# Optimization experiments

Measured on AMD Instinct MI355X. Metric: run time of the kernel, lower is better.

## Reference

```python
import jax, jax.numpy as jnp
import numpy as np

N, E, K_ORDER = 50000, 800000, 3
F_IN, H = 128, 128


def setup_inputs() -> dict:
    key = jax.random.key(0)
    ks = jax.random.split(key, 24)
    s = 0.05
    inp = {
        "x_t": jax.random.normal(ks[0], (N, F_IN), jnp.float32),
        "h_prev": jax.random.normal(ks[1], (N, H), jnp.float32),
        "c_prev": jax.random.normal(ks[2], (N, H), jnp.float32),
        "edge_weight": jax.random.uniform(ks[3], (E,), jnp.float32),
        "edge_index": jax.random.randint(ks[4], (2, E), 0, N, dtype=jnp.int64),
    }
    # Input->gate weight matrices W_* : (F, H)
    for i, nm in enumerate(["W_i", "W_f", "W_c", "W_o"]):
        inp[nm] = jax.random.normal(ks[5 + i], (F_IN, H), jnp.float32) * s
    # ChebConv weights theta_* : (K, H, H) applied to hidden state
    for i, nm in enumerate(["theta_i", "theta_f", "theta_c", "theta_o"]):
        inp[nm] = jax.random.normal(ks[9 + i], (K_ORDER, H, H), jnp.float32) * s
    # Gate biases (b_* of GCLSTM merged with the ChebConv bias; they add)
    for i, nm in enumerate(["b_i", "b_f", "b_c", "b_o"]):
        inp[nm] = jax.random.normal(ks[13 + i], (H,), jnp.float32) * s
    # Peephole weights w_c_* : (H,)
    for i, nm in enumerate(["w_ci", "w_cf", "w_co"]):
        inp[nm] = jax.random.normal(ks[17 + i], (H,), jnp.float32) * s
    return inp


def _cheb_norm(edge_index, edge_weight):
    # get_laplacian('sym') + lambda_max=2 scaling + add_self_loops(-1)
    # => L~ = -D^{-1/2} A D^{-1/2}  (zero diagonal)
    src, dst = edge_index[0], edge_index[1]
    deg = jax.ops.segment_sum(edge_weight, src, num_segments=N)
    dinv = jnp.where(deg > 0, jax.lax.rsqrt(jnp.maximum(deg, 1e-30)), 0.0)
    return src, dst, -edge_weight * dinv[src] * dinv[dst]


def _cheb_conv(x, theta, bias, src, dst, wn):
    # Chebyshev recursion: Tx0=x, Tx1=L~x, Tx_k = 2 L~ Tx_{k-1} - Tx_{k-2}
    def Lmul(v):
        return jax.ops.segment_sum(wn[:, None] * v[src], dst, num_segments=N)
    Tx0 = x
    Tx1 = Lmul(x)
    out = Tx0 @ theta[0] + Tx1 @ theta[1]
    for k in range(2, theta.shape[0]):
        Tx2 = 2.0 * Lmul(Tx1) - Tx0
        out = out + Tx2 @ theta[k]
        Tx0, Tx1 = Tx1, Tx2
    return out + bias


def reference(x_t, h_prev, c_prev, edge_weight, W_i, W_f, W_c, W_o,
              theta_i, theta_f, theta_c, theta_o, b_i, b_f, b_c, b_o,
              w_ci, w_cf, w_co, edge_index):
    src, dst, wn = _cheb_norm(edge_index, edge_weight)
    i = jax.nn.sigmoid(x_t @ W_i + _cheb_conv(h_prev, theta_i, b_i, src, dst, wn)
                       + w_ci * c_prev)
    f = jax.nn.sigmoid(x_t @ W_f + _cheb_conv(h_prev, theta_f, b_f, src, dst, wn)
                       + w_cf * c_prev)
    t = jnp.tanh(x_t @ W_c + _cheb_conv(h_prev, theta_c, b_c, src, dst, wn))
    c_t = f * c_prev + i * t
    o = jax.nn.sigmoid(x_t @ W_o + _cheb_conv(h_prev, theta_o, b_o, src, dst, wn)
                       + w_co * c_t)
    h_t = o * jnp.tanh(c_t)
    return (h_t, c_t)
```

## Files before the change

kernel.cpp:

```cpp
#include <hip/hip_runtime.h>

#define NN 50000
#define EE 800000
#define KC 64
#define EPC (EE / KC)
#define DEG_SCALE 4096.0f

typedef float f32x4 __attribute__((ext_vector_type(4)));
typedef short bf16x8 __attribute__((ext_vector_type(8)));
typedef unsigned short u16x8 __attribute__((ext_vector_type(8)));

__device__ __forceinline__ unsigned short f2bf(float f) {
  unsigned int u = __float_as_uint(f);
  u += 0x7fffu + ((u >> 16) & 1u);
  return (unsigned short)(u >> 16);
}
__device__ __forceinline__ float bf2f(unsigned short u) {
  return __uint_as_float(((unsigned int)u) << 16);
}

__device__ __forceinline__ void async_copy16(const void* g, void* l) {
  __builtin_amdgcn_global_load_lds(
      (const __attribute__((address_space(1))) unsigned int*)g,
      (__attribute__((address_space(3))) unsigned int*)l, 16, 0, 0);
}

__device__ __forceinline__ float fast_sig(float x) {
  return __builtin_amdgcn_rcpf(1.f + __expf(-x));
}
__device__ __forceinline__ float fast_tanh(float x) {
  return 1.f - 2.f * __builtin_amdgcn_rcpf(__expf(2.f * x) + 1.f);
}

__device__ __forceinline__ unsigned short* hslot2(char* o, long j) {
  return (unsigned short*)(o + (j >> 7) * 512 + (j & 127) * 2);
}
__device__ __forceinline__ void store8u16(char* o, long s, uint4 v) {
  *(uint4*)(o + (s >> 7) * 512 + (s & 127) * 2) = v;
}
#define CNT_SLOT0 3200000L
#define RANK_SLOT0 3200000L

__global__ __launch_bounds__(1024) void k_pre(
    const float* __restrict__ Wi, const float* __restrict__ Wf,
    const float* __restrict__ Wc, const float* __restrict__ Wo,
    const float* __restrict__ Ti, const float* __restrict__ Tf,
    const float* __restrict__ Tc, const float* __restrict__ To,
    unsigned short* __restrict__ bglob, const float* __restrict__ h,
    const float* __restrict__ x, char* __restrict__ outB,
    const int* __restrict__ src, const int* __restrict__ dst,
    const float* __restrict__ w) {
  __shared__ unsigned hist[25000];
  const int b = blockIdx.x, tid = threadIdx.x;
  char* cB = outB + (long)NN * 512;
  if (b < KC) {
    uint4* h4 = (uint4*)hist;
    const int base = b * EPC;
    for (int j = tid; j < 6250; j += 1024) h4[j] = (uint4){0u, 0u, 0u, 0u};
    __syncthreads();
    for (int k = tid; k < EPC; k += 1024) {
      const int e = base + k;
      const int d = dst[e];
      const int sh = (d & 1) * 16;
      const unsigned old = atomicAdd(&hist[d >> 1], 1u << sh);
      *hslot2(cB, RANK_SLOT0 + e) = (unsigned short)((old >> sh) & 0xffffu);
    }
    __syncthreads();
    for (int j = tid; j < 6250; j += 1024)
      store8u16(outB, CNT_SLOT0 + (long)b * NN + j * 8, h4[j]);
    __syncthreads();
    for (int j = tid; j < 6250; j += 1024) h4[j] = (uint4){0u, 0u, 0u, 0u};
    __syncthreads();
    for (int k = tid; k < EPC; k += 1024) {
      const int e = base + k;
      const int s = src[e];
      const unsigned q = (unsigned)__float2uint_rn(w[e] * DEG_SCALE);
      const int sh = (s & 1) * 16;
      atomicAdd(&hist[s >> 1], q << sh);
    }
    __syncthreads();
    for (int j = tid; j < 6250; j += 1024)
      store8u16(outB, (long)b * NN + j * 8, h4[j]);
  } else if (b < KC + 32) {
    const int t = (b - KC) * 1024 + tid;
    const int ks = t >> 11;
    const int cf = (t >> 6) & 31;
    const int lane = t & 63;
    const int wv = cf >> 3, hl = (cf >> 2) & 1, g = cf & 3;
    const int kg = lane >> 4, lm = lane & 15;
    const int hc = (wv * 2 + hl) * 16 + lm;
    const float* Wg = (g == 0) ? Wi : (g == 1) ? Wf : (g == 2) ? Wc : Wo;
    const float* Tg = (g == 0) ? Ti : (g == 1) ? Tf : (g == 2) ? Tc : To;
    u16x8 out;
#pragma unroll
    for (int dk = 0; dk < 8; ++dk) {
      const int k = ks * 32 + kg * 8 + dk;
      const int kb = k >> 7, r = k & 127;
      const float v = (kb == 0) ? Wg[r * 128 + hc] : Tg[(kb - 1) * 16384 + r * 128 + hc];
      out[dk] = f2bf(v);
    }
    *(u16x8*)(bglob + t * 8) = out;
  } else if (b < KC + 32 + 782) {
    const int i = (b - (KC + 32)) * 1024 + tid;
    if (i < 100000 * 8) {
      const float* hp = h + i * 8;
      const f32x4 v0 = *(const f32x4*)hp;
      const f32x4 v1 = *(const f32x4*)(hp + 4);
      u16x8 o;
#pragma unroll
      for (int e = 0; e < 4; ++e) o[e] = f2bf(v0[e]);
#pragma unroll
      for (int e = 0; e < 4; ++e) o[e + 4] = f2bf(v1[e]);
      *(u16x8*)(outB + (i >> 4) * 512 + 256 + (i & 15) * 16) = o;
    }
  } else {
    const int i = (b - (KC + 32 + 782)) * 1024 + tid;
    if (i < 100000 * 8) {
      const float* xp = x + i * 8;
      const f32x4 v0 = *(const f32x4*)xp;
      const f32x4 v1 = *(const f32x4*)(xp + 4);
      u16x8 o;
#pragma unroll
      for (int e = 0; e < 4; ++e) o[e] = f2bf(v0[e]);
#pragma unroll
      for (int e = 0; e < 4; ++e) o[e + 4] = f2bf(v1[e]);
      *(u16x8*)(cB + (i >> 4) * 512 + 256 + (i & 15) * 16) = o;
    }
  }
}

__global__ __launch_bounds__(256) void k_phase2(char* __restrict__ outB,
                                                float* __restrict__ dinv,
                                                int* __restrict__ wscnt) {
  char* cB = outB + (long)NN * 512;
  const int lane = threadIdx.x & 63;
  const int i = blockIdx.x * 4 + (threadIdx.x >> 6);
  const int c = lane;
  const int cnt_c = (int)*hslot2(outB, CNT_SLOT0 + (long)c * NN + i);
  const float deg_c = (float)*hslot2(outB, (long)c * NN + i);
  int x = cnt_c;
#pragma unroll
  for (int d = 1; d < 64; d <<= 1) {
    const int y = __shfl_up(x, d, 64);
    if (lane >= d) x += y;
  }
  *hslot2(cB, (long)c * NN + i) = (unsigned short)(x - cnt_c);
  float s = deg_c;
#pragma unroll
  for (int d = 1; d < 64; d <<= 1) s += __shfl_xor(s, d, 64);
  if (lane == 0) {
    s *= (1.0f / DEG_SCALE);
    dinv[i] = (s > 0.f) ? rsqrtf(fmaxf(s, 1e-30f)) : 0.f;
  }
  if (lane == 63) wscnt[i] = x;
}

__device__ __forceinline__ int block_scan_excl_256(int v, int* total) {
  __shared__ int wsum[4];
  const int tid = threadIdx.x;
  const int lane = tid & 63, wv = tid >> 6;
  int x = v;
#pragma unroll
  for (int d = 1; d < 64; d <<= 1) {
    const int y = __shfl_up(x, d, 64);
    if (lane >= d) x += y;
  }
  if (lane == 63) wsum[wv] = x;
  __syncthreads();
  int pre = 0, tot = 0;
#pragma unroll
  for (int u = 0; u < 4; ++u) {
    const int s = wsum[u];
    pre += (u < wv) ? s : 0;
    tot += s;
  }
  *total = tot;
  return pre + x - v;
}

__global__ void k_scan1(const int* __restrict__ wscnt, int* __restrict__ bsum) {
  const int i = blockIdx.x * 256 + threadIdx.x;
  const int v = (i < NN) ? wscnt[i] : 0;
  int tot;
  block_scan_excl_256(v, &tot);
  if (threadIdx.x == 0) bsum[blockIdx.x] = tot;
}

__global__ void k_scan2(const int* __restrict__ bsum, int* __restrict__ boff,
                        const int nb) {
  const int t = threadIdx.x;
  const int v = (t < nb) ? bsum[t] : 0;
  int tot;
  const int excl = block_scan_excl_256(v, &tot);
  if (t <= nb) boff[t] = excl;
}

__global__ void k_scan3(const int* __restrict__ cnt, const int* __restrict__ boff,
                        int* __restrict__ off) {
  const int i = blockIdx.x * 256 + threadIdx.x;
  const int v = (i < NN) ? cnt[i] : 0;
  int tot;
  const int excl = block_scan_excl_256(v, &tot) + boff[blockIdx.x];
  if (i < NN) off[i] = excl;
  if (i == NN) off[NN] = excl;
}

__global__ void k_edge2(const int* __restrict__ src, const int* __restrict__ dst,
                        const float* __restrict__ w, const float* __restrict__ dinv,
                        const int* __restrict__ off, char* __restrict__ outB,
                        int2* __restrict__ ed) {
  const int e = blockIdx.x * blockDim.x + threadIdx.x;
  if (e >= EE) return;
  char* cB = outB + (long)NN * 512;
  const int s = src[e], d = dst[e];
  const int c = e / EPC;
  const int p = off[d] + (int)*hslot2(cB, (long)c * NN + d) +
                (int)*hslot2(cB, RANK_SLOT0 + e);
  int2 rec;
  rec.x = s;
  rec.y = __float_as_int(-w[e] * dinv[s] * dinv[d]);
  ed[p] = rec;
}

__global__ __launch_bounds__(256) void k_gather(
    const char* __restrict__ vinB, const char* __restrict__ vsubB, const float alpha,
    const int* __restrict__ off, const int2* __restrict__ ed, char* __restrict__ voutB) {
  const int wid = threadIdx.x >> 6, lane = threadIdx.x & 63;
  const int node = blockIdx.x * 4 + wid;
  const int p0 = off[node], p1 = off[node + 1];
  const int lb = lane * 4;
  float ax0 = 0.f, ay0 = 0.f, ax1 = 0.f, ay1 = 0.f;
  float ax2 = 0.f, ay2 = 0.f, ax3 = 0.f, ay3 = 0.f;
  int p = p0;
  for (; p + 7 < p1; p += 8) {
    int2 E[8];
    unsigned V[8];
#pragma unroll
    for (int u = 0; u < 8; ++u) E[u] = ed[p + u];
#pragma unroll
    for (int u = 0; u < 8; ++u)
      V[u] = *(const unsigned*)(vinB + (long)E[u].x * 512 + lb);
#pragma unroll
    for (int u = 0; u < 8; ++u) {
      const float wv = __int_as_float(E[u].y);
      float* ax = (u & 3) == 0 ? &ax0 : (u & 3) == 1 ? &ax1 : (u & 3) == 2 ? &ax2 : &ax3;
      float* ay = (u & 3) == 0 ? &ay0 : (u & 3) == 1 ? &ay1 : (u & 3) == 2 ? &ay2 : &ay3;
      *ax = fmaf(wv, bf2f((unsigned short)V[u]), *ax);
      *ay = fmaf(wv, bf2f((unsigned short)(V[u] >> 16)), *ay);
    }
  }
  for (; p + 3 < p1; p += 4) {
    const int2 e0 = ed[p], e1 = ed[p + 1], e2 = ed[p + 2], e3 = ed[p + 3];
    const unsigned v0 = *(const unsigned*)(vinB + (long)e0.x * 512 + lb);
    const unsigned v1 = *(const unsigned*)(vinB + (long)e1.x * 512 + lb);
    const unsigned v2 = *(const unsigned*)(vinB + (long)e2.x * 512 + lb);
    const unsigned v3 = *(const unsigned*)(vinB + (long)e3.x * 512 + lb);
    const float w0 = __int_as_float(e0.y), w1 = __int_as_float(e1.y);
    const float w2 = __int_as_float(e2.y), w3 = __int_as_float(e3.y);
    ax0 = fmaf(w0, bf2f((unsigned short)v0), ax0);
    ay0 = fmaf(w0, bf2f((unsigned short)(v0 >> 16)), ay0);
    ax1 = fmaf(w1, bf2f((unsigned short)v1), ax1);
    ay1 = fmaf(w1, bf2f((unsigned short)(v1 >> 16)), ay1);
    ax2 = fmaf(w2, bf2f((unsigned short)v2), ax2);
    ay2 = fmaf(w2, bf2f((unsigned short)(v2 >> 16)), ay2);
    ax3 = fmaf(w3, bf2f((unsigned short)v3), ax3);
    ay3 = fmaf(w3, bf2f((unsigned short)(v3 >> 16)), ay3);
  }
  for (; p < p1; ++p) {
    const int2 e0 = ed[p];
    const unsigned v0 = *(const unsigned*)(vinB + (long)e0.x * 512 + lb);
    const float w0 = __int_as_float(e0.y);
    ax0 = fmaf(w0, bf2f((unsigned short)v0), ax0);
    ay0 = fmaf(w0, bf2f((unsigned short)(v0 >> 16)), ay0);
  }
  float rx = alpha * ((ax0 + ax1) + (ax2 + ax3));
  float ry = alpha * ((ay0 + ay1) + (ay2 + ay3));
  if (vsubB) {
    const unsigned s = *(const unsigned*)(vsubB + (long)node * 512 + lb);
    rx -= bf2f((unsigned short)s);
    ry -= bf2f((unsigned short)(s >> 16));
  }
  const unsigned ow = (unsigned)f2bf(rx) | ((unsigned)f2bf(ry) << 16);
  *(unsigned*)(voutB + (long)node * 512 + lb) = ow;
}

__global__ __launch_bounds__(512, 4) void k_gemm(
    const char* __restrict__ outB, const unsigned short* __restrict__ bglob,
    const float* __restrict__ c_prev,
    const float* __restrict__ b_i, const float* __restrict__ b_f,
    const float* __restrict__ b_c, const float* __restrict__ b_o,
    const float* __restrict__ w_ci, const float* __restrict__ w_cf,
    const float* __restrict__ w_co, float* __restrict__ h_out,
    float* __restrict__ c_out) {
  __shared__ char lds[65536];
  const int tid = threadIdx.x;
  const int lane = tid & 63;
  const int w = tid >> 6;
  const int kg = lane >> 4;
  const int lm = lane & 15;
  const int m0 = blockIdx.x * 64;

  const char* hB = outB;
  const char* cB = outB + (long)NN * 512;

  {
    const int t8 = tid & 255;
    const int rf = t8 >> 6, ln = t8 & 63;
    const int srow0 = m0 + rf * 16 + (ln & 15);
    const long srow = (srow0 < NN) ? srow0 : (NN - 1);
    const int schunk = (ln >> 4) * 16;
#pragma unroll
    for (int i = 0; i < 8; ++i) {
      const int ks = i * 2 + (tid >> 8);
      const char* base = (ks < 4) ? (cB + 256) : (ks < 8) ? (hB + 256) : (ks < 12) ? hB : cB;
      async_copy16(base + srow * 512 + (ks & 3) * 64 + schunk,
                   &lds[ks * 4096 + t8 * 16]);
    }
  }

  f32x4 acc[16];
#pragma unroll
  for (int i = 0; i < 16; ++i) acc[i] = (f32x4){0.f, 0.f, 0.f, 0.f};

  bf16x8 B[3][4];
  auto loadB = [&](int ks, bf16x8* bb) {
    const unsigned short* fp = bglob + ((ks * 32 + w * 4) * 64 + lane) * 8;
#pragma unroll
    for (int g = 0; g < 4; ++g) bb[g] = *(const bf16x8*)(fp + g * 512);
  };

  loadB(0, B[0]);
  loadB(1, B[1]);
  loadB(2, B[2]);

  __syncthreads();

#pragma unroll
  for (int ks = 0; ks < 16; ++ks) {
    const int m = ks % 3;
    bf16x8 a[4];
#pragma unroll
    for (int rf = 0; rf < 4; ++rf)
      a[rf] = *(const bf16x8*)(&lds[ks * 4096 + rf * 1024 + lane * 16]);
#pragma unroll
    for (int rf = 0; rf < 4; ++rf)
#pragma unroll
      for (int g = 0; g < 4; ++g)
        acc[rf * 4 + g] =
            __builtin_amdgcn_mfma_f32_16x16x32_bf16(a[rf], B[m][g], acc[rf * 4 + g], 0, 0, 0);
    if (ks + 3 < 16) loadB(ks + 3, B[m]);
  }

  const int hc = w * 16 + lm;
  const float bi = b_i[hc], bfv = b_f[hc], bc_ = b_c[hc], bo = b_o[hc];
  const float wci = w_ci[hc], wcf = w_cf[hc], wco = w_co[hc];
#pragma unroll
  for (int rf = 0; rf < 4; ++rf) {
#pragma unroll
    for (int reg = 0; reg < 4; ++reg) {
      const int node = m0 + rf * 16 + kg * 4 + reg;
      if (node < NN) {
        const float cp = c_prev[node * 128 + hc];
        const float pi = acc[rf * 4 + 0][reg] + bi + wci * cp;
        const float pf = acc[rf * 4 + 1][reg] + bfv + wcf * cp;
        const float pc = acc[rf * 4 + 2][reg] + bc_;
        const float po = acc[rf * 4 + 3][reg] + bo;
        const float ig = fast_sig(pi);
        const float fg = fast_sig(pf);
        const float ct = fg * cp + ig * fast_tanh(pc);
        const float og = fast_sig(po + wco * ct);
        h_out[node * 128 + hc] = og * fast_tanh(ct);
        c_out[node * 128 + hc] = ct;
      }
    }
  }
}


extern "C" void kernel_launch(void* const* d_in, const int* in_sizes, int n_in,
                              void* d_out, int out_size, void* d_ws, size_t ws_size,
                              hipStream_t stream) {
  const float* x_t    = (const float*)d_in[0];
  const float* h_prev = (const float*)d_in[1];
  const float* c_prev = (const float*)d_in[2];
  const float* ew     = (const float*)d_in[3];
  const int*   eidx   = (const int*)d_in[4];
  const float* Wi = (const float*)d_in[5];
  const float* Wf = (const float*)d_in[6];
  const float* Wc = (const float*)d_in[7];
  const float* Wo = (const float*)d_in[8];
  const float* Ti = (const float*)d_in[9];
  const float* Tf = (const float*)d_in[10];
  const float* Tc = (const float*)d_in[11];
  const float* To = (const float*)d_in[12];
  const float* bi = (const float*)d_in[13];
  const float* bf = (const float*)d_in[14];
  const float* bc = (const float*)d_in[15];
  const float* bo = (const float*)d_in[16];
  const float* wci = (const float*)d_in[17];
  const float* wcf = (const float*)d_in[18];
  const float* wco = (const float*)d_in[19];

  char* ws = (char*)d_ws;
  float* dinv  = (float*)(ws + 0);
  int*   wscnt = (int*)(ws + 200192);
  int*   off   = (int*)(ws + 400384);
  int*   bsum  = (int*)(ws + 601088);
  int*   boff  = (int*)(ws + 602112);
  int2*  ed    = (int2*)(ws + 603136);
  unsigned short* bglob = (unsigned short*)(ws + 7003136);

  char* outB = (char*)d_out;
  float* h_out = (float*)d_out;
  float* c_out = h_out + (long)NN * 128;

  const int* esrc = eidx;
  const int* edst = eidx + EE;

  k_pre<<<KC + 32 + 782 + 782, 1024, 0, stream>>>(
      Wi, Wf, Wc, Wo, Ti, Tf, Tc, To, bglob, h_prev, x_t, outB, esrc, edst, ew);
  k_phase2<<<12500, 256, 0, stream>>>(outB, dinv, wscnt);
  k_scan1<<<196, 256, 0, stream>>>(wscnt, bsum);
  k_scan2<<<1, 256, 0, stream>>>(bsum, boff, 196);
  k_scan3<<<196, 256, 0, stream>>>(wscnt, boff, off);
  k_edge2<<<3125, 256, 0, stream>>>(esrc, edst, ew, dinv, off, outB, ed);
  k_gather<<<12500, 256, 0, stream>>>(outB + 256, nullptr, 1.f, off, ed, outB);
  k_gather<<<12500, 256, 0, stream>>>(outB, outB + 256, 2.f, off, ed,
                                      outB + (long)NN * 512);
  k_gemm<<<782, 512, 0, stream>>>(outB, bglob, c_prev,
                                  bi, bf, bc, bo, wci, wcf, wco, h_out, c_out);
}
```

Baseline: 197.2 us.

## Make GEMM kernel persistent with double-buffered LDS panel prefetch

The gate GEMM/LSTM epilogue kernel becomes a persistent kernel: 256 blocks loop over the 782 row panels. While the current panel is being computed, the next panel's A tiles are staged asynchronously into a second 64KB LDS buffer. The A fragments are also double-buffered in registers across k-steps, and c_prev is prefetched before the MFMA loop. The aim is to hide global-to-LDS load latency and the tail of a partial wave. In exchange, LDS use doubles to 128KB per block, which limits occupancy to one block per CU, and the launch bound drops to 2.

```diff
diff --git a/kernel.cpp b/kernel.cpp
--- a/kernel.cpp
+++ b/kernel.cpp
@@ -5,6 +5,7 @@
 #define KC 64
 #define EPC (EE / KC)
 #define DEG_SCALE 4096.0f
+#define NPANEL 782
 
 typedef float f32x4 __attribute__((ext_vector_type(4)));
 typedef short bf16x8 __attribute__((ext_vector_type(8)));
@@ -284,7 +285,7 @@
   *(unsigned*)(voutB + (long)node * 512 + lb) = ow;
 }
 
-__global__ __launch_bounds__(512, 4) void k_gemm(
+__global__ __launch_bounds__(512, 2) void k_gemm(
     const char* __restrict__ outB, const unsigned short* __restrict__ bglob,
     const float* __restrict__ c_prev,
     const float* __restrict__ b_i, const float* __restrict__ b_f,
@@ -292,35 +293,32 @@
     const float* __restrict__ w_ci, const float* __restrict__ w_cf,
     const float* __restrict__ w_co, float* __restrict__ h_out,
     float* __restrict__ c_out) {
-  __shared__ char lds[65536];
+  __shared__ char lds[2][65536];
   const int tid = threadIdx.x;
   const int lane = tid & 63;
   const int w = tid >> 6;
   const int kg = lane >> 4;
   const int lm = lane & 15;
-  const int m0 = blockIdx.x * 64;
 
   const char* hB = outB;
   const char* cB = outB + (long)NN * 512;
 
-  {
-    const int t8 = tid & 255;
-    const int rf = t8 >> 6, ln = t8 & 63;
-    const int srow0 = m0 + rf * 16 + (ln & 15);
+  const int t8 = tid & 255;
+  const int sks0 = tid >> 8;
+  const int srowoff = (t8 >> 6) * 16 + (t8 & 15);
+  const int schunk = ((t8 & 63) >> 4) * 16;
+
+  auto stageA = [&](int p, int buf) {
+    const int srow0 = p * 64 + srowoff;
     const long srow = (srow0 < NN) ? srow0 : (NN - 1);
-    const int schunk = (ln >> 4) * 16;
 #pragma unroll
     for (int i = 0; i < 8; ++i) {
-      const int ks = i * 2 + (tid >> 8);
+      const int ks = i * 2 + sks0;
       const char* base = (ks < 4) ? (cB + 256) : (ks < 8) ? (hB + 256) : (ks < 12) ? hB : cB;
       async_copy16(base + srow * 512 + (ks & 3) * 64 + schunk,
-                   &lds[ks * 4096 + t8 * 16]);
-    }
-  }
-
-  f32x4 acc[16];
-#pragma unroll
-  for (int i = 0; i < 16; ++i) acc[i] = (f32x4){0.f, 0.f, 0.f, 0.f};
+                   &lds[buf][ks * 4096 + t8 * 16]);
+    }
+  };
 
   bf16x8 B[3][4];
   auto loadB = [&](int ks, bf16x8* bb) {
@@ -329,50 +327,78 @@
     for (int g = 0; g < 4; ++g) bb[g] = *(const bf16x8*)(fp + g * 512);
   };
 
-  loadB(0, B[0]);
-  loadB(1, B[1]);
-  loadB(2, B[2]);
-
-  __syncthreads();
-
-#pragma unroll
-  for (int ks = 0; ks < 16; ++ks) {
-    const int m = ks % 3;
-    bf16x8 a[4];
-#pragma unroll
-    for (int rf = 0; rf < 4; ++rf)
-      a[rf] = *(const bf16x8*)(&lds[ks * 4096 + rf * 1024 + lane * 16]);
-#pragma unroll
-    for (int rf = 0; rf < 4; ++rf)
-#pragma unroll
-      for (int g = 0; g < 4; ++g)
-        acc[rf * 4 + g] =
-            __builtin_amdgcn_mfma_f32_16x16x32_bf16(a[rf], B[m][g], acc[rf * 4 + g], 0, 0, 0);
-    if (ks + 3 < 16) loadB(ks + 3, B[m]);
-  }
-
   const int hc = w * 16 + lm;
   const float bi = b_i[hc], bfv = b_f[hc], bc_ = b_c[hc], bo = b_o[hc];
   const float wci = w_ci[hc], wcf = w_cf[hc], wco = w_co[hc];
-#pragma unroll
-  for (int rf = 0; rf < 4; ++rf) {
-#pragma unroll
-    for (int reg = 0; reg < 4; ++reg) {
-      const int node = m0 + rf * 16 + kg * 4 + reg;
-      if (node < NN) {
-        const float cp = c_prev[node * 128 + hc];
-        const float pi = acc[rf * 4 + 0][reg] + bi + wci * cp;
-        const float pf = acc[rf * 4 + 1][reg] + bfv + wcf * cp;
-        const float pc = acc[rf * 4 + 2][reg] + bc_;
-        const float po = acc[rf * 4 + 3][reg] + bo;
-        const float ig = fast_sig(pi);
-        const float fg = fast_sig(pf);
-        const float ct = fg * cp + ig * fast_tanh(pc);
-        const float og = fast_sig(po + wco * ct);
-        h_out[node * 128 + hc] = og * fast_tanh(ct);
-        c_out[node * 128 + hc] = ct;
+
+  int buf = 0;
+  stageA(blockIdx.x, 0);
+
+  for (int p = blockIdx.x; p < NPANEL; p += 256) {
+    __syncthreads();
+    if (p + 256 < NPANEL) stageA(p + 256, buf ^ 1);
+    const int m0 = p * 64;
+    float cp[16];
+#pragma unroll
+    for (int rf = 0; rf < 4; ++rf)
+#pragma unroll
+      for (int reg = 0; reg < 4; ++reg) {
+        int node = m0 + rf * 16 + kg * 4 + reg;
+        if (node >= NN) node = NN - 1;
+        cp[rf * 4 + reg] = c_prev[node * 128 + hc];
       }
-    }
+    loadB(0, B[0]);
+    loadB(1, B[1]);
+    loadB(2, B[2]);
+
+    f32x4 acc[16];
+#pragma unroll
+    for (int i = 0; i < 16; ++i) acc[i] = (f32x4){0.f, 0.f, 0.f, 0.f};
+
+    bf16x8 a0[4], a1[4];
+#pragma unroll
+    for (int rf = 0; rf < 4; ++rf)
+      a0[rf] = *(const bf16x8*)(&lds[buf][rf * 1024 + lane * 16]);
+#pragma unroll
+    for (int ks = 0; ks < 16; ++ks) {
+      bf16x8* ac = (ks & 1) ? a1 : a0;
+      bf16x8* an = (ks & 1) ? a0 : a1;
+      if (ks < 15) {
+#pragma unroll
+        for (int rf = 0; rf < 4; ++rf)
+          an[rf] = *(const bf16x8*)(&lds[buf][(ks + 1) * 4096 + rf * 1024 + lane * 16]);
+      }
+      const int m = ks % 3;
+#pragma unroll
+      for (int rf = 0; rf < 4; ++rf)
+#pragma unroll
+        for (int g = 0; g < 4; ++g)
+          acc[rf * 4 + g] = __builtin_amdgcn_mfma_f32_16x16x32_bf16(
+              ac[rf], B[m][g], acc[rf * 4 + g], 0, 0, 0);
+      if (ks + 3 < 16) loadB(ks + 3, B[m]);
+    }
+
+#pragma unroll
+    for (int rf = 0; rf < 4; ++rf) {
+#pragma unroll
+      for (int reg = 0; reg < 4; ++reg) {
+        const int node = m0 + rf * 16 + kg * 4 + reg;
+        if (node < NN) {
+          const float cpv = cp[rf * 4 + reg];
+          const float pi = acc[rf * 4 + 0][reg] + bi + wci * cpv;
+          const float pf = acc[rf * 4 + 1][reg] + bfv + wcf * cpv;
+          const float pc = acc[rf * 4 + 2][reg] + bc_;
+          const float po = acc[rf * 4 + 3][reg] + bo;
+          const float ig = fast_sig(pi);
+          const float fg = fast_sig(pf);
+          const float ct = fg * cpv + ig * fast_tanh(pc);
+          const float og = fast_sig(po + wco * ct);
+          h_out[node * 128 + hc] = og * fast_tanh(ct);
+          c_out[node * 128 + hc] = ct;
+        }
+      }
+    }
+    buf ^= 1;
   }
 }
 
@@ -427,6 +453,6 @@
   k_gather<<<12500, 256, 0, stream>>>(outB + 256, nullptr, 1.f, off, ed, outB);
   k_gather<<<12500, 256, 0, stream>>>(outB, outB + 256, 2.f, off, ed,
                                       outB + (long)NN * 512);
-  k_gemm<<<782, 512, 0, stream>>>(outB, bglob, c_prev,
+  k_gemm<<<256, 512, 0, stream>>>(outB, bglob, c_prev,
                                   bi, bf, bc, bo, wci, wcf, wco, h_out, c_out);
 }
```

Result: slower. 241.1 us (+22.3%).

## Redistribute h/x bf16 conversion into later kernels and deepen GEMM B prefetch

Applied to the files above, without the earlier changes.

Moves the h_prev bf16 conversion out of the histogram pre-kernel into extra blocks of k_phase2, and the x_t conversion into extra blocks of the first gather. The aim is to shorten the critical histogram kernel and fill idle slots in later kernels. The GEMM B-operand ring buffer grows from three to four stages, and c_prev loads are hoisted before the MFMA loop to hide their latency. This costs more registers and may lower occupancy. The x conversion must still finish before the second gather reads that region.

```diff
diff --git a/kernel.cpp b/kernel.cpp
--- a/kernel.cpp
+++ b/kernel.cpp
@@ -5,6 +5,7 @@
 #define KC 64
 #define EPC (EE / KC)
 #define DEG_SCALE 4096.0f
+#define NPANEL 782
 
 typedef float f32x4 __attribute__((ext_vector_type(4)));
 typedef short bf16x8 __attribute__((ext_vector_type(8)));
@@ -46,8 +47,7 @@
     const float* __restrict__ Wc, const float* __restrict__ Wo,
     const float* __restrict__ Ti, const float* __restrict__ Tf,
     const float* __restrict__ Tc, const float* __restrict__ To,
-    unsigned short* __restrict__ bglob, const float* __restrict__ h,
-    const float* __restrict__ x, char* __restrict__ outB,
+    unsigned short* __restrict__ bglob, char* __restrict__ outB,
     const int* __restrict__ src, const int* __restrict__ dst,
     const float* __restrict__ w) {
   __shared__ unsigned hist[25000];
@@ -81,7 +81,7 @@
     __syncthreads();
     for (int j = tid; j < 6250; j += 1024)
       store8u16(outB, (long)b * NN + j * 8, h4[j]);
-  } else if (b < KC + 32) {
+  } else {
     const int t = (b - KC) * 1024 + tid;
     const int ks = t >> 11;
     const int cf = (t >> 6) & 31;
@@ -100,59 +100,48 @@
       out[dk] = f2bf(v);
     }
     *(u16x8*)(bglob + t * 8) = out;
-  } else if (b < KC + 32 + 782) {
-    const int i = (b - (KC + 32)) * 1024 + tid;
-    if (i < 100000 * 8) {
-      const float* hp = h + i * 8;
-      const f32x4 v0 = *(const f32x4*)hp;
-      const f32x4 v1 = *(const f32x4*)(hp + 4);
-      u16x8 o;
-#pragma unroll
-      for (int e = 0; e < 4; ++e) o[e] = f2bf(v0[e]);
-#pragma unroll
-      for (int e = 0; e < 4; ++e) o[e + 4] = f2bf(v1[e]);
-      *(u16x8*)(outB + (i >> 4) * 512 + 256 + (i & 15) * 16) = o;
-    }
-  } else {
-    const int i = (b - (KC + 32 + 782)) * 1024 + tid;
-    if (i < 100000 * 8) {
-      const float* xp = x + i * 8;
-      const f32x4 v0 = *(const f32x4*)xp;
-      const f32x4 v1 = *(const f32x4*)(xp + 4);
-      u16x8 o;
-#pragma unroll
-      for (int e = 0; e < 4; ++e) o[e] = f2bf(v0[e]);
-#pragma unroll
-      for (int e = 0; e < 4; ++e) o[e + 4] = f2bf(v1[e]);
-      *(u16x8*)(cB + (i >> 4) * 512 + 256 + (i & 15) * 16) = o;
-    }
   }
 }
 
 __global__ __launch_bounds__(256) void k_phase2(char* __restrict__ outB,
                                                 float* __restrict__ dinv,
-                                                int* __restrict__ wscnt) {
+                                                int* __restrict__ wscnt,
+                                                const float* __restrict__ h) {
   char* cB = outB + (long)NN * 512;
-  const int lane = threadIdx.x & 63;
-  const int i = blockIdx.x * 4 + (threadIdx.x >> 6);
-  const int c = lane;
-  const int cnt_c = (int)*hslot2(outB, CNT_SLOT0 + (long)c * NN + i);
-  const float deg_c = (float)*hslot2(outB, (long)c * NN + i);
-  int x = cnt_c;
-#pragma unroll
-  for (int d = 1; d < 64; d <<= 1) {
-    const int y = __shfl_up(x, d, 64);
-    if (lane >= d) x += y;
-  }
-  *hslot2(cB, (long)c * NN + i) = (unsigned short)(x - cnt_c);
-  float s = deg_c;
-#pragma unroll
-  for (int d = 1; d < 64; d <<= 1) s += __shfl_xor(s, d, 64);
-  if (lane == 0) {
-    s *= (1.0f / DEG_SCALE);
-    dinv[i] = (s > 0.f) ? rsqrtf(fmaxf(s, 1e-30f)) : 0.f;
-  }
-  if (lane == 63) wscnt[i] = x;
+  const int b = blockIdx.x;
+  if (b < 12500) {
+    const int lane = threadIdx.x & 63;
+    const int i = b * 4 + (threadIdx.x >> 6);
+    const int c = lane;
+    const int cnt_c = (int)*hslot2(outB, CNT_SLOT0 + (long)c * NN + i);
+    const float deg_c = (float)*hslot2(outB, (long)c * NN + i);
+    int x = cnt_c;
+#pragma unroll
+    for (int d = 1; d < 64; d <<= 1) {
+      const int y = __shfl_up(x, d, 64);
+      if (lane >= d) x += y;
+    }
+    *hslot2(cB, (long)c * NN + i) = (unsigned short)(x - cnt_c);
+    float s = deg_c;
+#pragma unroll
+    for (int d = 1; d < 64; d <<= 1) s += __shfl_xor(s, d, 64);
+    if (lane == 0) {
+      s *= (1.0f / DEG_SCALE);
+      dinv[i] = (s > 0.f) ? rsqrtf(fmaxf(s, 1e-30f)) : 0.f;
+    }
+    if (lane == 63) wscnt[i] = x;
+  } else {
+    const int i = (b - 12500) * 256 + threadIdx.x;
+    const float* hp = h + i * 8;
+    const f32x4 v0 = *(const f32x4*)hp;
+    const f32x4 v1 = *(const f32x4*)(hp + 4);
+    u16x8 o;
+#pragma unroll
+    for (int e = 0; e < 4; ++e) o[e] = f2bf(v0[e]);
+#pragma unroll
+    for (int e = 0; e < 4; ++e) o[e + 4] = f2bf(v1[e]);
+    *(u16x8*)(outB + (i >> 4) * 512 + 256 + (i & 15) * 16) = o;
+  }
 }
 
 __device__ __forceinline__ int block_scan_excl_256(int v, int* total) {
@@ -224,7 +213,21 @@
 
 __global__ __launch_bounds__(256) void k_gather(
     const char* __restrict__ vinB, const char* __restrict__ vsubB, const float alpha,
-    const int* __restrict__ off, const int2* __restrict__ ed, char* __restrict__ voutB) {
+    const int* __restrict__ off, const int2* __restrict__ ed, char* __restrict__ voutB,
+    const float* __restrict__ xconv, char* __restrict__ xdst) {
+  if (blockIdx.x >= 12500) {
+    const int i = (blockIdx.x - 12500) * 256 + threadIdx.x;
+    const float* xp = xconv + i * 8;
+    const f32x4 v0 = *(const f32x4*)xp;
+    const f32x4 v1 = *(const f32x4*)(xp + 4);
+    u16x8 o;
+#pragma unroll
+    for (int e = 0; e < 4; ++e) o[e] = f2bf(v0[e]);
+#pragma unroll
+    for (int e = 0; e < 4; ++e) o[e + 4] = f2bf(v1[e]);
+    *(u16x8*)(xdst + (i >> 4) * 512 + 256 + (i & 15) * 16) = o;
+    return;
+  }
   const int wid = threadIdx.x >> 6, lane = threadIdx.x & 63;
   const int node = blockIdx.x * 4 + wid;
   const int p0 = off[node], p1 = off[node + 1];
@@ -322,7 +325,7 @@
 #pragma unroll
   for (int i = 0; i < 16; ++i) acc[i] = (f32x4){0.f, 0.f, 0.f, 0.f};
 
-  bf16x8 B[3][4];
+  bf16x8 B[4][4];
   auto loadB = [&](int ks, bf16x8* bb) {
     const unsigned short* fp = bglob + ((ks * 32 + w * 4) * 64 + lane) * 8;
 #pragma unroll
@@ -335,9 +338,21 @@
 
   __syncthreads();
 
+  const int hc = w * 16 + lm;
+  float cp[16];
+#pragma unroll
+  for (int rf = 0; rf < 4; ++rf)
+#pragma unroll
+    for (int reg = 0; reg < 4; ++reg) {
+      int node = m0 + rf * 16 + kg * 4 + reg;
+      if (node >= NN) node = NN - 1;
+      cp[rf * 4 + reg] = c_prev[node * 128 + hc];
+    }
+  loadB(3, B[3]);
+
 #pragma unroll
   for (int ks = 0; ks < 16; ++ks) {
-    const int m = ks % 3;
+    const int m = ks & 3;
     bf16x8 a[4];
 #pragma unroll
     for (int rf = 0; rf < 4; ++rf)
@@ -348,10 +363,9 @@
       for (int g = 0; g < 4; ++g)
         acc[rf * 4 + g] =
             __builtin_amdgcn_mfma_f32_16x16x32_bf16(a[rf], B[m][g], acc[rf * 4 + g], 0, 0, 0);
-    if (ks + 3 < 16) loadB(ks + 3, B[m]);
-  }
-
-  const int hc = w * 16 + lm;
+    if (ks + 4 < 16) loadB(ks + 4, B[m]);
+  }
+
   const float bi = b_i[hc], bfv = b_f[hc], bc_ = b_c[hc], bo = b_o[hc];
   const float wci = w_ci[hc], wcf = w_cf[hc], wco = w_co[hc];
 #pragma unroll
@@ -360,14 +374,14 @@
     for (int reg = 0; reg < 4; ++reg) {
       const int node = m0 + rf * 16 + kg * 4 + reg;
       if (node < NN) {
-        const float cp = c_prev[node * 128 + hc];
-        const float pi = acc[rf * 4 + 0][reg] + bi + wci * cp;
-        const float pf = acc[rf * 4 + 1][reg] + bfv + wcf * cp;
+        const float cpv = cp[rf * 4 + reg];
+        const float pi = acc[rf * 4 + 0][reg] + bi + wci * cpv;
+        const float pf = acc[rf * 4 + 1][reg] + bfv + wcf * cpv;
         const float pc = acc[rf * 4 + 2][reg] + bc_;
         const float po = acc[rf * 4 + 3][reg] + bo;
         const float ig = fast_sig(pi);
         const float fg = fast_sig(pf);
-        const float ct = fg * cp + ig * fast_tanh(pc);
+        const float ct = fg * cpv + ig * fast_tanh(pc);
         const float og = fast_sig(po + wco * ct);
         h_out[node * 128 + hc] = og * fast_tanh(ct);
         c_out[node * 128 + hc] = ct;
@@ -417,16 +431,17 @@
   const int* esrc = eidx;
   const int* edst = eidx + EE;
 
-  k_pre<<<KC + 32 + 782 + 782, 1024, 0, stream>>>(
-      Wi, Wf, Wc, Wo, Ti, Tf, Tc, To, bglob, h_prev, x_t, outB, esrc, edst, ew);
-  k_phase2<<<12500, 256, 0, stream>>>(outB, dinv, wscnt);
+  k_pre<<<KC + 32, 1024, 0, stream>>>(Wi, Wf, Wc, Wo, Ti, Tf, Tc, To, bglob,
+                                      outB, esrc, edst, ew);
+  k_phase2<<<12500 + 3125, 256, 0, stream>>>(outB, dinv, wscnt, h_prev);
   k_scan1<<<196, 256, 0, stream>>>(wscnt, bsum);
   k_scan2<<<1, 256, 0, stream>>>(bsum, boff, 196);
   k_scan3<<<196, 256, 0, stream>>>(wscnt, boff, off);
   k_edge2<<<3125, 256, 0, stream>>>(esrc, edst, ew, dinv, off, outB, ed);
-  k_gather<<<12500, 256, 0, stream>>>(outB + 256, nullptr, 1.f, off, ed, outB);
+  k_gather<<<12500 + 3125, 256, 0, stream>>>(outB + 256, nullptr, 1.f, off, ed, outB,
+                                             x_t, outB + (long)NN * 512);
   k_gather<<<12500, 256, 0, stream>>>(outB, outB + 256, 2.f, off, ed,
-                                      outB + (long)NN * 512);
-  k_gemm<<<782, 512, 0, stream>>>(outB, bglob, c_prev,
-                                  bi, bf, bc, bo, wci, wcf, wco, h_out, c_out);
-}
+                                      outB + (long)NN * 512, nullptr, nullptr);
+  k_gemm<<<NPANEL, 512, 0, stream>>>(outB, bglob, c_prev,
+                                     bi, bf, bc, bo, wci, wcf, wco, h_out, c_out);
+}
```

After: 197.9 us. About the same (+0.4%).
